# Optimization experiments

Hardware: AMD Instinct MI355X
Metric: run time of the kernel (lower is better)

The kernel has to match this reference:

```python
import jax, jax.numpy as jnp
import numpy as np

KERNEL_SIZE = 37  # int((6*20-7)//3) = 37, already odd
PAD = (KERNEL_SIZE - 1) // 2  # 18


def moving_avg(x):
    """Edge-replicated moving average along token axis. x: [B, T, C]."""
    front = jnp.repeat(x[:, :1, :], PAD, axis=1)
    end = jnp.repeat(x[:, -1:, :], PAD, axis=1)
    xp = jnp.concatenate([front, x, end], axis=1)  # [B, T+2*PAD, C]
    cs = jnp.cumsum(xp, axis=1)
    cs = jnp.concatenate([jnp.zeros_like(cs[:, :1, :]), cs], axis=1)
    # window sums: length (T+2*PAD+1) - KERNEL_SIZE = T
    return (cs[:, KERNEL_SIZE:, :] - cs[:, :-KERNEL_SIZE, :]) / KERNEL_SIZE


def setup_inputs() -> dict:
    key = jax.random.key(0)
    ks = jax.random.split(key, 5)
    B, T, Cin, Cout = 4096, 17, 512, 512
    scale = 1.0 / np.sqrt(Cin)
    x = jax.random.normal(ks[0], (B, T, Cin), dtype=jnp.float32)
    W_seasonal = jax.random.uniform(ks[1], (T, Cout, Cin), jnp.float32, -scale, scale)
    b_seasonal = jax.random.uniform(ks[2], (T, Cout), jnp.float32, -scale, scale)
    W_trend = jax.random.uniform(ks[3], (T, Cout, Cin), jnp.float32, -scale, scale)
    b_trend = jax.random.uniform(ks[4], (T, Cout), jnp.float32, -scale, scale)
    return {"x": x, "W_seasonal": W_seasonal, "b_seasonal": b_seasonal,
            "W_trend": W_trend, "b_trend": b_trend}


def reference(x, W_seasonal, b_seasonal, W_trend, b_trend):
    trend = moving_avg(x)            # [B, T, Cin]
    seasonal = x - trend             # [B, T, Cin]
    # per-token (grouped) linear layers as one batched einsum
    s_out = jnp.einsum('btc,tdc->btd', seasonal, W_seasonal) + b_seasonal[None]
    t_out = jnp.einsum('btc,tdc->btd', trend, W_trend) + b_trend[None]
    return s_out + t_out
```

## Files before the change

### kernel.cpp

```cpp
#include <hip/hip_runtime.h>
#include <stdint.h>

#define B_N 4096
#define T_N 17
#define C_N 512
#define KTOT 1024

typedef __bf16 bf16x8 __attribute__((ext_vector_type(8)));
typedef float  f32x4  __attribute__((ext_vector_type(4)));

__device__ __forceinline__ unsigned short f2b(float f){
  unsigned u = __float_as_uint(f);
  return (unsigned short)((u + 0x7fffu + ((u >> 16) & 1u)) >> 16);
}
__device__ __forceinline__ unsigned pk2(float a, float b){
  return (unsigned)f2b(a) | ((unsigned)f2b(b) << 16);
}

__device__ __forceinline__ void gll16(const void* g, void* l){
  __builtin_amdgcn_global_load_lds(
      (const __attribute__((address_space(1))) unsigned int*)g,
      (__attribute__((address_space(3))) unsigned int*)l, 16, 0, 0);
}

#define BAR()   __builtin_amdgcn_s_barrier()
#define VMC(n)  do{ asm volatile("s_waitcnt vmcnt(" #n ")" ::: "memory"); \
                    __builtin_amdgcn_sched_barrier(0); }while(0)
#define FENCE() asm volatile("" ::: "memory")

__global__ __launch_bounds__(256) void prep_w(
    const float* __restrict__ Ws, const float* __restrict__ Wt,
    unsigned short* __restrict__ wcat)
{
  const size_t i8 = ((size_t)blockIdx.x * 256 + threadIdx.x) * 8;
  const int t   = (int)(i8 >> 18);
  const int rem = (int)(i8 & 262143);
  const int d   = rem >> 9;
  const int c   = rem & 511;
  float4 a0 = *(const float4*)(Ws + i8);
  float4 a1 = *(const float4*)(Ws + i8 + 4);
  float4 b0 = *(const float4*)(Wt + i8);
  float4 b1 = *(const float4*)(Wt + i8 + 4);
  uint4 oa, od;
  oa.x = pk2(a0.x, a0.y); oa.y = pk2(a0.z, a0.w);
  oa.z = pk2(a1.x, a1.y); oa.w = pk2(a1.z, a1.w);
  od.x = pk2(b0.x - a0.x, b0.y - a0.y); od.y = pk2(b0.z - a0.z, b0.w - a0.w);
  od.z = pk2(b1.x - a1.x, b1.y - a1.y); od.w = pk2(b1.z - a1.z, b1.w - a1.w);
  unsigned short* base = wcat + ((size_t)(t * C_N + d)) * KTOT + c;
  *(uint4*)base = oa;
  *(uint4*)(base + C_N) = od;
}

__global__ __launch_bounds__(256) void prep_bsum(
    const float* __restrict__ bs, const float* __restrict__ bt, float* __restrict__ o)
{
  const int i = blockIdx.x * 256 + threadIdx.x;
  o[i] = bs[i] + bt[i];
}

__global__ __launch_bounds__(256) void prep_a(
    const float* __restrict__ x, unsigned short* __restrict__ acat)
{
  const int idx = blockIdx.x * 256 + threadIdx.x;
  const int b = idx >> 6;
  const int c = (idx & 63) << 3;
  const float* xp = x + (size_t)b * (T_N * C_N) + c;
  float s[8] = {0,0,0,0,0,0,0,0};
  float f0[8], fl[8];
#pragma unroll
  for (int tt = 0; tt < T_N; ++tt){
    float4 w0 = *(const float4*)(xp + (size_t)tt * C_N);
    float4 w1 = *(const float4*)(xp + (size_t)tt * C_N + 4);
    float f[8] = {w0.x, w0.y, w0.z, w0.w, w1.x, w1.y, w1.z, w1.w};
    uint4 o;
    o.x = pk2(f[0],f[1]); o.y = pk2(f[2],f[3]);
    o.z = pk2(f[4],f[5]); o.w = pk2(f[6],f[7]);
    *(uint4*)(acat + ((size_t)tt * B_N + b) * KTOT + c) = o;
    if (tt == 0){
#pragma unroll
      for (int i=0;i<8;++i) f0[i] = f[i];
    }
    if (tt == T_N-1){
#pragma unroll
      for (int i=0;i<8;++i) fl[i] = f[i];
    }
#pragma unroll
    for (int i=0;i<8;++i) s[i] += f[i];
  }
  const float inv = 1.0f / 37.0f;
  float uu[8], vv[8];
#pragma unroll
  for (int i=0;i<8;++i){
    uu[i] = (s[i] + 18.0f * f0[i] + 2.0f * fl[i]) * inv;
    vv[i] = (fl[i] - f0[i]) * inv;
  }
#pragma unroll
  for (int tt = 0; tt < T_N; ++tt){
    const float tfv = (float)tt;
    float tr[8];
#pragma unroll
    for (int i=0;i<8;++i) tr[i] = fmaf(tfv, vv[i], uu[i]);
    uint4 o;
    o.x = pk2(tr[0],tr[1]); o.y = pk2(tr[2],tr[3]);
    o.z = pk2(tr[4],tr[5]); o.w = pk2(tr[6],tr[7]);
    *(uint4*)(acat + ((size_t)tt * B_N + b) * KTOT + C_N + c) = o;
  }
}

__global__ __launch_bounds__(512, 2) void gemm8(
    const unsigned short* __restrict__ acat,
    const unsigned short* __restrict__ wcat,
    const float* __restrict__ bsum,
    float* __restrict__ out)
{
  __shared__ alignas(16) unsigned short A_lds[2][256][64];
  __shared__ alignas(16) unsigned short B_lds[2][256][64];

  const int tid = threadIdx.x;
  const int bid = blockIdx.x;
  const int wg = (bid & 7) * 68 + (bid >> 3);
  const int t  = wg >> 5;
  const int mt = (wg >> 1) & 15;
  const int nt = wg & 1;
  const int m0 = mt << 8;
  const int n0 = nt << 8;

  const int lane = tid & 63;
  const int wave = tid >> 6;
  const int wr = wave >> 2;
  const int wc = wave & 3;
  const int lr = lane & 15;
  const int g  = lane >> 4;

  const int row0 = tid >> 3;
  const int cc0  = tid & 7;
  const int cswz = ((cc0 ^ (row0 & 7)) << 3);
  const unsigned short* gA0 = acat + ((size_t)t * B_N + m0 + row0) * KTOT + cswz;
  const unsigned short* gB0 = wcat + ((size_t)t * C_N + n0 + row0) * KTOT + cswz;
  unsigned short* lA0 = &A_lds[0][row0][cc0 << 3];
  unsigned short* lB0 = &B_lds[0][row0][cc0 << 3];

  auto stageA = [&](int bb, int kt){
#pragma unroll
    for (int r = 0; r < 4; ++r)
      gll16(gA0 + (size_t)kt * 64 + r * 65536, lA0 + bb * 16384 + r * 4096);
  };
  auto stageB = [&](int bb, int kt){
#pragma unroll
    for (int r = 0; r < 4; ++r)
      gll16(gB0 + (size_t)kt * 64 + r * 65536, lB0 + bb * 16384 + r * 4096);
  };

  const int sw  = lr & 7;
  const int ca0 = (( g     ) ^ sw) << 3;
  const int ca1 = ((4 | g  ) ^ sw) << 3;
  const unsigned short* Arow = &A_lds[0][wr * 128 + lr][0];
  const unsigned short* Brow = &B_lds[0][wc * 64  + lr][0];

  f32x4 acc[8][4];
#pragma unroll
  for (int i=0;i<8;++i)
#pragma unroll
    for (int j=0;j<4;++j){ f32x4 z = {0.f,0.f,0.f,0.f}; acc[i][j] = z; }

  auto rdA4 = [&](bf16x8 (&dst)[4][2], int bb, int mih){
    const unsigned short* p = Arow + bb * 16384 + mih * 1024;
#pragma unroll
    for (int mi=0;mi<4;++mi){
      dst[mi][0] = *(const bf16x8*)(p + mi * 1024 + ca0);
      dst[mi][1] = *(const bf16x8*)(p + mi * 1024 + ca1);
    }
  };
  auto rdB2 = [&](bf16x8 (&dst)[2][2], int bb, int nih){
    const unsigned short* p = Brow + bb * 16384 + nih * 1024;
#pragma unroll
    for (int ni=0;ni<2;++ni){
      dst[ni][0] = *(const bf16x8*)(p + ni * 1024 + ca0);
      dst[ni][1] = *(const bf16x8*)(p + ni * 1024 + ca1);
    }
  };

  stageB(0, 0); stageA(0, 0);
  stageB(1, 1); stageA(1, 1);
  VMC(8);
  BAR();

#pragma unroll 1
  for (int it = 0; it < 16; ++it){
    const int bb = it & 1;
    bf16x8 b01[2][2], b23[2][2], aL[4][2], aH[4][2];

    rdB2(b01, bb, 0);
    rdB2(b23, bb, 2);
    rdA4(aL, bb, 0);

    __builtin_amdgcn_s_setprio(1);
#pragma unroll
    for (int mi=0;mi<4;++mi){
      if (mi == 2) rdA4(aH, bb, 4);
#pragma unroll
      for (int ni=0;ni<2;++ni){
        acc[mi][ni]   = __builtin_amdgcn_mfma_f32_16x16x32_bf16(aL[mi][0], b01[ni][0], acc[mi][ni],0,0,0);
        acc[mi][ni]   = __builtin_amdgcn_mfma_f32_16x16x32_bf16(aL[mi][1], b01[ni][1], acc[mi][ni],0,0,0);
        acc[mi][2+ni] = __builtin_amdgcn_mfma_f32_16x16x32_bf16(aL[mi][0], b23[ni][0], acc[mi][2+ni],0,0,0);
        acc[mi][2+ni] = __builtin_amdgcn_mfma_f32_16x16x32_bf16(aL[mi][1], b23[ni][1], acc[mi][2+ni],0,0,0);
      }
    }
#pragma unroll
    for (int mi=0;mi<4;++mi){
#pragma unroll
      for (int ni=0;ni<2;++ni){
        acc[4+mi][ni]   = __builtin_amdgcn_mfma_f32_16x16x32_bf16(aH[mi][0], b01[ni][0], acc[4+mi][ni],0,0,0);
        acc[4+mi][ni]   = __builtin_amdgcn_mfma_f32_16x16x32_bf16(aH[mi][1], b01[ni][1], acc[4+mi][ni],0,0,0);
        acc[4+mi][2+ni] = __builtin_amdgcn_mfma_f32_16x16x32_bf16(aH[mi][0], b23[ni][0], acc[4+mi][2+ni],0,0,0);
        acc[4+mi][2+ni] = __builtin_amdgcn_mfma_f32_16x16x32_bf16(aH[mi][1], b23[ni][1], acc[4+mi][2+ni],0,0,0);
      }
    }
    __builtin_amdgcn_s_setprio(0);

    FENCE();
    BAR();
    if (it < 14){
      stageB(bb, it + 2);
      stageA(bb, it + 2);
      VMC(8);
    } else if (it == 14){
      VMC(0);
    }
    BAR();
  }

  float bias[4];
#pragma unroll
  for (int ni=0;ni<4;++ni)
    bias[ni] = bsum[(size_t)t * C_N + n0 + wc*64 + ni*16 + lr];

#pragma unroll
  for (int mi=0;mi<8;++mi){
#pragma unroll
    for (int rr=0;rr<4;++rr){
      const int m = m0 + wr*128 + mi*16 + g*4 + rr;
      float* op = out + ((size_t)m * T_N + t) * C_N + n0 + wc*64 + lr;
#pragma unroll
      for (int ni=0;ni<4;++ni)
        op[ni*16] = acc[mi][ni][rr] + bias[ni];
    }
  }
}

extern "C" void kernel_launch(void* const* d_in, const int* in_sizes, int n_in,
                              void* d_out, int out_size, void* d_ws, size_t ws_size,
                              hipStream_t stream)
{
  const float* x   = (const float*)d_in[0];
  const float* Wsl = (const float*)d_in[1];
  const float* bsl = (const float*)d_in[2];
  const float* Wtr = (const float*)d_in[3];
  const float* btr = (const float*)d_in[4];
  float* out = (float*)d_out;

  const size_t WCAT_BYTES = (size_t)T_N * C_N * KTOT * 2;
  const size_t BS_BYTES   = (size_t)T_N * C_N * 4;
  char* ws = (char*)d_ws;
  unsigned short* wcat = (unsigned short*)ws;
  float*          bsum = (float*)(ws + WCAT_BYTES);
  unsigned short* acat = (unsigned short*)(ws + WCAT_BYTES + BS_BYTES);

  prep_w  <<<dim3(2176), dim3(256), 0, stream>>>(Wsl, Wtr, wcat);
  prep_bsum<<<dim3(34),  dim3(256), 0, stream>>>(bsl, btr, bsum);
  prep_a  <<<dim3(1024), dim3(256), 0, stream>>>(x, acat);
  gemm8   <<<dim3(544),  dim3(512), 0, stream>>>(acat, wcat, bsum, out);
  (void)in_sizes; (void)n_in; (void)out_size; (void)ws_size;
}
```

Baseline: 423.9 us.

## Shrink GEMM tile to 128x128 with 4 waves and fold bias add into epilogue

Replaces the 256x256-tile, 8-wave GEMM with a 128x128-tile, 4-wave kernel launched over 2176 workgroups, with each wave computing a 64x64 sub-tile. The workgroup-to-tile mapping and LDS staging offsets change to match. The separate bias-sum kernel is dropped: the epilogue now reads both bias vectors and adds them, which removes one launch. Smaller tiles give more workgroups to balance across CUs, at the cost of less operand reuse per byte loaded and more total global/L2 traffic for A and W.

```diff
diff --git a/kernel.cpp b/kernel.cpp
--- a/kernel.cpp
+++ b/kernel.cpp
@@ -51,13 +51,6 @@
   *(uint4*)(base + C_N) = od;
 }
 
-__global__ __launch_bounds__(256) void prep_bsum(
-    const float* __restrict__ bs, const float* __restrict__ bt, float* __restrict__ o)
-{
-  const int i = blockIdx.x * 256 + threadIdx.x;
-  o[i] = bs[i] + bt[i];
-}
-
 __global__ __launch_bounds__(256) void prep_a(
     const float* __restrict__ x, unsigned short* __restrict__ acat)
 {
@@ -107,28 +100,30 @@
   }
 }
 
-__global__ __launch_bounds__(512, 2) void gemm8(
+__global__ __launch_bounds__(256, 2) void gemm4(
     const unsigned short* __restrict__ acat,
     const unsigned short* __restrict__ wcat,
-    const float* __restrict__ bsum,
+    const float* __restrict__ bs,
+    const float* __restrict__ bt,
     float* __restrict__ out)
 {
-  __shared__ alignas(16) unsigned short A_lds[2][256][64];
-  __shared__ alignas(16) unsigned short B_lds[2][256][64];
+  __shared__ alignas(16) unsigned short A_lds[2][128][64];
+  __shared__ alignas(16) unsigned short B_lds[2][128][64];
 
   const int tid = threadIdx.x;
   const int bid = blockIdx.x;
-  const int wg = (bid & 7) * 68 + (bid >> 3);
-  const int t  = wg >> 5;
-  const int mt = (wg >> 1) & 15;
-  const int nt = wg & 1;
-  const int m0 = mt << 8;
-  const int n0 = nt << 8;
+  const int wg = (bid & 7) * 272 + (bid >> 3);
+  const int t  = wg >> 7;
+  const int rm = wg & 127;
+  const int mt = rm >> 2;
+  const int nt = rm & 3;
+  const int m0 = mt << 7;
+  const int n0 = nt << 7;
 
   const int lane = tid & 63;
   const int wave = tid >> 6;
-  const int wr = wave >> 2;
-  const int wc = wave & 3;
+  const int wr = wave >> 1;
+  const int wc = wave & 1;
   const int lr = lane & 15;
   const int g  = lane >> 4;
 
@@ -137,92 +132,66 @@
   const int cswz = ((cc0 ^ (row0 & 7)) << 3);
   const unsigned short* gA0 = acat + ((size_t)t * B_N + m0 + row0) * KTOT + cswz;
   const unsigned short* gB0 = wcat + ((size_t)t * C_N + n0 + row0) * KTOT + cswz;
-  unsigned short* lA0 = &A_lds[0][row0][cc0 << 3];
-  unsigned short* lB0 = &B_lds[0][row0][cc0 << 3];
-
-  auto stageA = [&](int bb, int kt){
+  unsigned short* lA0 = &A_lds[0][0][0] + tid * 8;
+  unsigned short* lB0 = &B_lds[0][0][0] + tid * 8;
+
+  auto stage = [&](int bb, int kt){
 #pragma unroll
     for (int r = 0; r < 4; ++r)
-      gll16(gA0 + (size_t)kt * 64 + r * 65536, lA0 + bb * 16384 + r * 4096);
+      gll16(gB0 + (size_t)kt * 64 + r * 32768, lB0 + bb * 8192 + r * 2048);
+#pragma unroll
+    for (int r = 0; r < 4; ++r)
+      gll16(gA0 + (size_t)kt * 64 + r * 32768, lA0 + bb * 8192 + r * 2048);
   };
-  auto stageB = [&](int bb, int kt){
-#pragma unroll
-    for (int r = 0; r < 4; ++r)
-      gll16(gB0 + (size_t)kt * 64 + r * 65536, lB0 + bb * 16384 + r * 4096);
-  };
 
   const int sw  = lr & 7;
-  const int ca0 = (( g     ) ^ sw) << 3;
-  const int ca1 = ((4 | g  ) ^ sw) << 3;
-  const unsigned short* Arow = &A_lds[0][wr * 128 + lr][0];
-  const unsigned short* Brow = &B_lds[0][wc * 64  + lr][0];
-
-  f32x4 acc[8][4];
-#pragma unroll
-  for (int i=0;i<8;++i)
+  const int ca0 = (( g    ) ^ sw) << 3;
+  const int ca1 = ((4 | g ) ^ sw) << 3;
+  const unsigned short* Arow = &A_lds[0][wr * 64 + lr][0];
+  const unsigned short* Brow = &B_lds[0][wc * 64 + lr][0];
+
+  f32x4 acc[4][4];
+#pragma unroll
+  for (int i=0;i<4;++i)
 #pragma unroll
     for (int j=0;j<4;++j){ f32x4 z = {0.f,0.f,0.f,0.f}; acc[i][j] = z; }
 
-  auto rdA4 = [&](bf16x8 (&dst)[4][2], int bb, int mih){
-    const unsigned short* p = Arow + bb * 16384 + mih * 1024;
-#pragma unroll
-    for (int mi=0;mi<4;++mi){
-      dst[mi][0] = *(const bf16x8*)(p + mi * 1024 + ca0);
-      dst[mi][1] = *(const bf16x8*)(p + mi * 1024 + ca1);
-    }
-  };
-  auto rdB2 = [&](bf16x8 (&dst)[2][2], int bb, int nih){
-    const unsigned short* p = Brow + bb * 16384 + nih * 1024;
-#pragma unroll
-    for (int ni=0;ni<2;++ni){
-      dst[ni][0] = *(const bf16x8*)(p + ni * 1024 + ca0);
-      dst[ni][1] = *(const bf16x8*)(p + ni * 1024 + ca1);
-    }
-  };
-
-  stageB(0, 0); stageA(0, 0);
-  stageB(1, 1); stageA(1, 1);
+  stage(0, 0);
+  stage(1, 1);
   VMC(8);
   BAR();
 
 #pragma unroll 1
   for (int it = 0; it < 16; ++it){
     const int bb = it & 1;
-    bf16x8 b01[2][2], b23[2][2], aL[4][2], aH[4][2];
-
-    rdB2(b01, bb, 0);
-    rdB2(b23, bb, 2);
-    rdA4(aL, bb, 0);
+    bf16x8 af[4][2], bf[4][2];
+#pragma unroll
+    for (int i=0;i<4;++i){
+      const unsigned short* pB = Brow + bb * 8192 + i * 1024;
+      bf[i][0] = *(const bf16x8*)(pB + ca0);
+      bf[i][1] = *(const bf16x8*)(pB + ca1);
+    }
+#pragma unroll
+    for (int i=0;i<4;++i){
+      const unsigned short* pA = Arow + bb * 8192 + i * 1024;
+      af[i][0] = *(const bf16x8*)(pA + ca0);
+      af[i][1] = *(const bf16x8*)(pA + ca1);
+    }
 
     __builtin_amdgcn_s_setprio(1);
 #pragma unroll
-    for (int mi=0;mi<4;++mi){
-      if (mi == 2) rdA4(aH, bb, 4);
-#pragma unroll
-      for (int ni=0;ni<2;++ni){
-        acc[mi][ni]   = __builtin_amdgcn_mfma_f32_16x16x32_bf16(aL[mi][0], b01[ni][0], acc[mi][ni],0,0,0);
-        acc[mi][ni]   = __builtin_amdgcn_mfma_f32_16x16x32_bf16(aL[mi][1], b01[ni][1], acc[mi][ni],0,0,0);
-        acc[mi][2+ni] = __builtin_amdgcn_mfma_f32_16x16x32_bf16(aL[mi][0], b23[ni][0], acc[mi][2+ni],0,0,0);
-        acc[mi][2+ni] = __builtin_amdgcn_mfma_f32_16x16x32_bf16(aL[mi][1], b23[ni][1], acc[mi][2+ni],0,0,0);
+    for (int mi=0;mi<4;++mi)
+#pragma unroll
+      for (int ni=0;ni<4;++ni){
+        acc[mi][ni] = __builtin_amdgcn_mfma_f32_16x16x32_bf16(af[mi][0], bf[ni][0], acc[mi][ni],0,0,0);
+        acc[mi][ni] = __builtin_amdgcn_mfma_f32_16x16x32_bf16(af[mi][1], bf[ni][1], acc[mi][ni],0,0,0);
       }
-    }
-#pragma unroll
-    for (int mi=0;mi<4;++mi){
-#pragma unroll
-      for (int ni=0;ni<2;++ni){
-        acc[4+mi][ni]   = __builtin_amdgcn_mfma_f32_16x16x32_bf16(aH[mi][0], b01[ni][0], acc[4+mi][ni],0,0,0);
-        acc[4+mi][ni]   = __builtin_amdgcn_mfma_f32_16x16x32_bf16(aH[mi][1], b01[ni][1], acc[4+mi][ni],0,0,0);
-        acc[4+mi][2+ni] = __builtin_amdgcn_mfma_f32_16x16x32_bf16(aH[mi][0], b23[ni][0], acc[4+mi][2+ni],0,0,0);
-        acc[4+mi][2+ni] = __builtin_amdgcn_mfma_f32_16x16x32_bf16(aH[mi][1], b23[ni][1], acc[4+mi][2+ni],0,0,0);
-      }
-    }
     __builtin_amdgcn_s_setprio(0);
 
     FENCE();
     BAR();
     if (it < 14){
-      stageB(bb, it + 2);
-      stageA(bb, it + 2);
+      stage(bb, it + 2);
       VMC(8);
     } else if (it == 14){
       VMC(0);
@@ -232,14 +201,16 @@
 
   float bias[4];
 #pragma unroll
-  for (int ni=0;ni<4;++ni)
-    bias[ni] = bsum[(size_t)t * C_N + n0 + wc*64 + ni*16 + lr];
-
-#pragma unroll
-  for (int mi=0;mi<8;++mi){
+  for (int ni=0;ni<4;++ni){
+    const size_t bi = (size_t)t * C_N + n0 + wc*64 + ni*16 + lr;
+    bias[ni] = bs[bi] + bt[bi];
+  }
+
+#pragma unroll
+  for (int mi=0;mi<4;++mi){
 #pragma unroll
     for (int rr=0;rr<4;++rr){
-      const int m = m0 + wr*128 + mi*16 + g*4 + rr;
+      const int m = m0 + wr*64 + mi*16 + g*4 + rr;
       float* op = out + ((size_t)m * T_N + t) * C_N + n0 + wc*64 + lr;
 #pragma unroll
       for (int ni=0;ni<4;++ni)
@@ -260,15 +231,12 @@
   float* out = (float*)d_out;
 
   const size_t WCAT_BYTES = (size_t)T_N * C_N * KTOT * 2;
-  const size_t BS_BYTES   = (size_t)T_N * C_N * 4;
   char* ws = (char*)d_ws;
   unsigned short* wcat = (unsigned short*)ws;
-  float*          bsum = (float*)(ws + WCAT_BYTES);
-  unsigned short* acat = (unsigned short*)(ws + WCAT_BYTES + BS_BYTES);
-
-  prep_w  <<<dim3(2176), dim3(256), 0, stream>>>(Wsl, Wtr, wcat);
-  prep_bsum<<<dim3(34),  dim3(256), 0, stream>>>(bsl, btr, bsum);
-  prep_a  <<<dim3(1024), dim3(256), 0, stream>>>(x, acat);
-  gemm8   <<<dim3(544),  dim3(512), 0, stream>>>(acat, wcat, bsum, out);
+  unsigned short* acat = (unsigned short*)(ws + WCAT_BYTES);
+
+  prep_w <<<dim3(2176), dim3(256), 0, stream>>>(Wsl, Wtr, wcat);
+  prep_a <<<dim3(1024), dim3(256), 0, stream>>>(x, acat);
+  gemm4  <<<dim3(2176), dim3(256), 0, stream>>>(acat, wcat, bsl, btr, out);
   (void)in_sizes; (void)n_in; (void)out_size; (void)ws_size;
 }
```

Measured after the change: 413.4 us. 2.5% less time.
